# Performance work log

Measured on AMD Instinct MI355X. Metric: run time of the kernel, lower is better.

Reference implementation:

```python
import jax, jax.numpy as jnp
import numpy as np

N_NODES = 100_000
N_EDGES = 3_200_000
N_GRAPHS = 8
HIDDEN = 16
DEPTH = 10
IN_CH = 7  # pos(3)+norm(3)+curve(1); spline=False -> SAGEConv path
EPS = 1e-5
LOC = IN_CH + HIDDEN * DEPTH  # 167
PIN = LOC + 1024              # 1191


def _bn(x, g, b):
    # BatchNorm1d over nodes, training-mode statistics (deterministic)
    m = jnp.mean(x, 0)
    v = jnp.var(x, 0)
    return g * (x - m) * jax.lax.rsqrt(v + EPS) + b


def _sage(x, src, dst, w_nb, b_nb, w_rt):
    # PyG SAGEConv: mean-aggregate neighbor features then linear, plus root linear
    agg = jax.ops.segment_sum(x[src], dst, num_segments=N_NODES)
    cnt = jax.ops.segment_sum(jnp.ones((src.shape[0],), x.dtype), dst, num_segments=N_NODES)
    agg = agg / jnp.maximum(cnt, 1.0)[:, None]
    return agg @ w_nb + b_nb + x @ w_rt


def _mlp_block(x, w, b, g, be):
    # Lin -> ReLU -> BN (dropout is identity in eval mode)
    return _bn(jax.nn.relu(x @ w + b), g, be)


def _forward(pos, norm, curve, edge_index, batch, w_nb0, b_nb0, w_rt0, w_nb, b_nb, w_rt, bn_g, bn_b, g_w1, g_b1, g_g1, g_be1, g_w2, g_b2, g_g2, g_be2, g_w3, g_b3, g_g3, g_be3, p_w1, p_b1, p_g1, p_be1, p_w2, p_b2, p_g2, p_be2, p_w3, p_b3, p_g3, p_be3, out_w, out_b):
    src, dst = edge_index[0], edge_index[1]
    x_sage = jnp.concatenate([pos, norm, curve], axis=1)  # [N, 7]
    x = x_sage
    feats = []
    for i in range(DEPTH):
        if i == 0:
            h = _sage(x, src, dst, w_nb0, b_nb0, w_rt0)
        else:
            h = _sage(x, src, dst, w_nb[i - 1], b_nb[i - 1], w_rt[i - 1])
        x = jax.nn.elu(_bn(h, bn_g[i], bn_b[i]))
        feats.append(x)
    local_features = jnp.concatenate(feats + [x_sage], axis=1)  # [N, 167]
    g = _mlp_block(local_features, g_w1, g_b1, g_g1, g_be1)
    g = _mlp_block(g, g_w2, g_b2, g_g2, g_be2)
    g = _mlp_block(g, g_w3, g_b3, g_g3, g_be3)  # [N, 1024]
    pooled = jax.ops.segment_max(g, batch, num_segments=N_GRAPHS)  # [B, 1024]
    global_features = pooled[batch]  # broadcast back per node (== repeat_interleave)
    p = jnp.concatenate([local_features, global_features], axis=1)  # [N, 1191]
    p = _mlp_block(p, p_w1, p_b1, p_g1, p_be1)
    p = _mlp_block(p, p_w2, p_b2, p_g2, p_be2)
    p = _mlp_block(p, p_w3, p_b3, p_g3, p_be3)
    return p @ out_w + out_b  # [N, 1]


def setup_inputs() -> dict:
    key = jax.random.key(0)
    ks = iter(jax.random.split(key, 64))
    f32 = jnp.float32

    def W(i, o):
        return jax.random.normal(next(ks), (i, o), f32) * (1.0 / np.sqrt(i))

    pos = jax.random.normal(next(ks), (N_NODES, 3), f32)
    norm = jax.random.normal(next(ks), (N_NODES, 3), f32)
    curve = jax.random.normal(next(ks), (N_NODES, 1), f32)
    edge_index = jax.random.randint(next(ks), (2, N_EDGES), 0, N_NODES, dtype=jnp.int32)
    batch = jnp.sort(jax.random.randint(next(ks), (N_NODES,), 0, N_GRAPHS, dtype=jnp.int32))

    w_nb0 = W(IN_CH, HIDDEN); b_nb0 = jnp.zeros((HIDDEN,), f32); w_rt0 = W(IN_CH, HIDDEN)
    w_nb = jax.random.normal(next(ks), (DEPTH - 1, HIDDEN, HIDDEN), f32) * (1.0 / np.sqrt(HIDDEN))
    b_nb = jnp.zeros((DEPTH - 1, HIDDEN), f32)
    w_rt = jax.random.normal(next(ks), (DEPTH - 1, HIDDEN, HIDDEN), f32) * (1.0 / np.sqrt(HIDDEN))
    bn_g = jnp.ones((DEPTH, HIDDEN), f32); bn_b = jnp.zeros((DEPTH, HIDDEN), f32)

    g_w1 = W(LOC, 256); g_b1 = jnp.zeros((256,), f32); g_g1 = jnp.ones((256,), f32); g_be1 = jnp.zeros((256,), f32)
    g_w2 = W(256, 512); g_b2 = jnp.zeros((512,), f32); g_g2 = jnp.ones((512,), f32); g_be2 = jnp.zeros((512,), f32)
    g_w3 = W(512, 1024); g_b3 = jnp.zeros((1024,), f32); g_g3 = jnp.ones((1024,), f32); g_be3 = jnp.zeros((1024,), f32)

    p_w1 = W(PIN, 512); p_b1 = jnp.zeros((512,), f32); p_g1 = jnp.ones((512,), f32); p_be1 = jnp.zeros((512,), f32)
    p_w2 = W(512, 256); p_b2 = jnp.zeros((256,), f32); p_g2 = jnp.ones((256,), f32); p_be2 = jnp.zeros((256,), f32)
    p_w3 = W(256, 128); p_b3 = jnp.zeros((128,), f32); p_g3 = jnp.ones((128,), f32); p_be3 = jnp.zeros((128,), f32)

    out_w = W(128, 1); out_b = jnp.zeros((1,), f32)

    return dict(pos=pos, norm=norm, curve=curve, edge_index=edge_index, batch=batch,
                w_nb0=w_nb0, b_nb0=b_nb0, w_rt0=w_rt0, w_nb=w_nb, b_nb=b_nb, w_rt=w_rt,
                bn_g=bn_g, bn_b=bn_b,
                g_w1=g_w1, g_b1=g_b1, g_g1=g_g1, g_be1=g_be1,
                g_w2=g_w2, g_b2=g_b2, g_g2=g_g2, g_be2=g_be2,
                g_w3=g_w3, g_b3=g_b3, g_g3=g_g3, g_be3=g_be3,
                p_w1=p_w1, p_b1=p_b1, p_g1=p_g1, p_be1=p_be1,
                p_w2=p_w2, p_b2=p_b2, p_g2=p_g2, p_be2=p_be2,
                p_w3=p_w3, p_b3=p_b3, p_g3=p_g3, p_be3=p_be3,
                out_w=out_w, out_b=out_b)


def reference(pos, norm, curve, edge_index, batch, w_nb0, b_nb0, w_rt0, w_nb, b_nb, w_rt, bn_g, bn_b, g_w1, g_b1, g_g1, g_be1, g_w2, g_b2, g_g2, g_be2, g_w3, g_b3, g_g3, g_be3, p_w1, p_b1, p_g1, p_be1, p_w2, p_b2, p_g2, p_be2, p_w3, p_b3, p_g3, p_be3, out_w, out_b):
    return _forward(pos, norm, curve, edge_index, batch, w_nb0, b_nb0, w_rt0, w_nb, b_nb, w_rt, bn_g, bn_b, g_w1, g_b1, g_g1, g_be1, g_w2, g_b2, g_g2, g_be2, g_w3, g_b3, g_g3, g_be3, p_w1, p_b1, p_g1, p_be1, p_w2, p_b2, p_g2, p_be2, p_w3, p_b3, p_g3, p_be3, out_w, out_b)
```

## Files before the change

### kernel.cpp

```cpp
#include <hip/hip_runtime.h>
#include <math.h>

#define NN 100000
#define NE 3200000
#define NGRAPH 8
#define DEPTH 10
#define LOCC 167
#define LOCP 176
#define BNEPS 1e-5f

typedef _Float16 h16;
typedef _Float16 h8 __attribute__((ext_vector_type(8)));
typedef float f4 __attribute__((ext_vector_type(4)));

__device__ __forceinline__ float h2f(h16 v) { return (float)v; }
__device__ __forceinline__ h16 f2h(float v) { return (h16)v; }

__global__ void k_count(const int* __restrict__ dst, int* __restrict__ cnt) {
    int e = blockIdx.x * 256 + threadIdx.x;
    atomicAdd(&cnt[dst[e]], 1);
}

__global__ __launch_bounds__(256) void k_scan1(const int* __restrict__ cnt,
                                               int* __restrict__ row_start,
                                               int* __restrict__ bsum) {
    int i = blockIdx.x * 256 + threadIdx.x;
    int lane = threadIdx.x & 63, wid = threadIdx.x >> 6;
    int v = (i < NN) ? cnt[i] : 0;
    int orig = v;
    #pragma unroll
    for (int off = 1; off < 64; off <<= 1) {
        int u = __shfl_up(v, off, 64);
        if (lane >= off) v += u;
    }
    __shared__ int ws[4];
    if (lane == 63) ws[wid] = v;
    __syncthreads();
    int add = 0;
    for (int w = 0; w < wid; w++) add += ws[w];
    v += add;
    if (i < NN) row_start[i] = v - orig;
    if (threadIdx.x == 255) bsum[blockIdx.x] = v;
}

__global__ __launch_bounds__(512) void k_scan2(int* __restrict__ bsum, int nb) {
    int t = threadIdx.x, lane = t & 63, wid = t >> 6;
    int v = (t < nb) ? bsum[t] : 0;
    int orig = v;
    #pragma unroll
    for (int off = 1; off < 64; off <<= 1) {
        int u = __shfl_up(v, off, 64);
        if (lane >= off) v += u;
    }
    __shared__ int ws[8];
    if (lane == 63) ws[wid] = v;
    __syncthreads();
    int add = 0;
    for (int w = 0; w < wid; w++) add += ws[w];
    v += add;
    if (t < nb) bsum[t] = v - orig;
}

__global__ void k_scan3(const int* __restrict__ cnt, int* __restrict__ row_start,
                        const int* __restrict__ bsum, float* __restrict__ inv_cnt) {
    int i = blockIdx.x * 256 + threadIdx.x;
    if (i < NN) {
        row_start[i] += bsum[blockIdx.x];
        inv_cnt[i] = 1.0f / fmaxf((float)cnt[i], 1.0f);
    }
    if (i == 0) row_start[NN] = NE;
}

__global__ void k_fill(const int* __restrict__ src, const int* __restrict__ dst,
                       const int* __restrict__ row_start, int* __restrict__ cursor,
                       int* __restrict__ csr) {
    int e = blockIdx.x * 256 + threadIdx.x;
    int d = dst[e];
    int o = atomicAdd(&cursor[d], 1);
    csr[row_start[d] + o] = src[e];
}

__global__ void k_build_x0(const float* __restrict__ pos, const float* __restrict__ nrm,
                           const float* __restrict__ cur, float* __restrict__ x,
                           h16* __restrict__ local) {
    int n = blockIdx.x * 256 + threadIdx.x;
    if (n >= NN) return;
    float v[7];
    v[0] = pos[n * 3 + 0]; v[1] = pos[n * 3 + 1]; v[2] = pos[n * 3 + 2];
    v[3] = nrm[n * 3 + 0]; v[4] = nrm[n * 3 + 1]; v[5] = nrm[n * 3 + 2];
    v[6] = cur[n];
    float* xr = x + (size_t)n * 16;
    #pragma unroll
    for (int c = 0; c < 7; c++) xr[c] = v[c];
    #pragma unroll
    for (int c = 7; c < 16; c++) xr[c] = 0.f;
    h16* lr = local + (size_t)n * LOCP;
    #pragma unroll
    for (int c = 0; c < 7; c++) lr[160 + c] = f2h(v[c]);
    #pragma unroll
    for (int c = LOCC; c < LOCP; c++) lr[c] = f2h(0.f);
}

__global__ __launch_bounds__(256) void k_sage(
    const float* __restrict__ x, const int* __restrict__ row_start,
    const int* __restrict__ csr, const float* __restrict__ inv_cnt,
    const float* __restrict__ w_nb, const float* __restrict__ b_nb,
    const float* __restrict__ w_rt, int kin,
    float* __restrict__ h_out, float* __restrict__ ssum, float* __restrict__ ssq) {
    const float4* x4 = (const float4*)x;
    int t = threadIdx.x, lane = t & 63, wid = t >> 6;
    int n = blockIdx.x * 64 + wid * 16 + (lane >> 2);
    int q = lane & 3;
    bool valid = n < NN;
    int s = 0, e = 0;
    if (valid) { s = row_start[n]; e = row_start[n + 1]; }
    float ax = 0.f, ay = 0.f, az = 0.f, aw = 0.f;
    int j = s;
    for (; j + 3 < e; j += 4) {
        int a0 = csr[j], a1 = csr[j + 1], a2 = csr[j + 2], a3 = csr[j + 3];
        float4 v0 = x4[a0 * 4 + q];
        float4 v1 = x4[a1 * 4 + q];
        float4 v2 = x4[a2 * 4 + q];
        float4 v3 = x4[a3 * 4 + q];
        ax += (v0.x + v1.x) + (v2.x + v3.x);
        ay += (v0.y + v1.y) + (v2.y + v3.y);
        az += (v0.z + v1.z) + (v2.z + v3.z);
        aw += (v0.w + v1.w) + (v2.w + v3.w);
    }
    for (; j < e; j++) {
        float4 v = x4[csr[j] * 4 + q];
        ax += v.x; ay += v.y; az += v.z; aw += v.w;
    }
    float ic = valid ? inv_cnt[n] : 0.f;
    float agg[4] = {ax * ic, ay * ic, az * ic, aw * ic};
    float xn[4] = {0.f, 0.f, 0.f, 0.f};
    if (valid) {
        float4 v = x4[n * 4 + q];
        xn[0] = v.x; xn[1] = v.y; xn[2] = v.z; xn[3] = v.w;
    }
    float hc0 = 0.f, hc1 = 0.f, hc2 = 0.f, hc3 = 0.f;
    #pragma unroll
    for (int r = 0; r < 4; r++) {
        int kq = (q + r) & 3;
        int srcl = (lane & 60) | kq;
        float av[4], xv[4];
        #pragma unroll
        for (int c = 0; c < 4; c++) {
            av[c] = __shfl(agg[c], srcl, 64);
            xv[c] = __shfl(xn[c], srcl, 64);
        }
        #pragma unroll
        for (int kk = 0; kk < 4; kk++) {
            int k = kq * 4 + kk;
            if (k < kin) {
                float4 wn4 = *(const float4*)&w_nb[k * 16 + 4 * q];
                float4 wr4 = *(const float4*)&w_rt[k * 16 + 4 * q];
                hc0 = fmaf(av[kk], wn4.x, hc0); hc0 = fmaf(xv[kk], wr4.x, hc0);
                hc1 = fmaf(av[kk], wn4.y, hc1); hc1 = fmaf(xv[kk], wr4.y, hc1);
                hc2 = fmaf(av[kk], wn4.z, hc2); hc2 = fmaf(xv[kk], wr4.z, hc2);
                hc3 = fmaf(av[kk], wn4.w, hc3); hc3 = fmaf(xv[kk], wr4.w, hc3);
            }
        }
    }
    float4 b4 = *(const float4*)&b_nb[4 * q];
    hc0 += b4.x; hc1 += b4.y; hc2 += b4.z; hc3 += b4.w;
    if (!valid) { hc0 = 0.f; hc1 = 0.f; hc2 = 0.f; hc3 = 0.f; }
    else {
        *(float4*)&h_out[(size_t)n * 16 + 4 * q] = make_float4(hc0, hc1, hc2, hc3);
    }
    float s0 = hc0, s1 = hc1, s2 = hc2, s3 = hc3;
    float q0 = hc0 * hc0, q1 = hc1 * hc1, q2 = hc2 * hc2, q3 = hc3 * hc3;
    #pragma unroll
    for (int off = 4; off < 64; off <<= 1) {
        s0 += __shfl_xor(s0, off, 64); s1 += __shfl_xor(s1, off, 64);
        s2 += __shfl_xor(s2, off, 64); s3 += __shfl_xor(s3, off, 64);
        q0 += __shfl_xor(q0, off, 64); q1 += __shfl_xor(q1, off, 64);
        q2 += __shfl_xor(q2, off, 64); q3 += __shfl_xor(q3, off, 64);
    }
    if (lane < 4) {
        int slot = blockIdx.x & 63;
        float* ps = &ssum[slot * 16 + 4 * lane];
        float* pq = &ssq[slot * 16 + 4 * lane];
        atomicAdd(ps + 0, s0); atomicAdd(ps + 1, s1);
        atomicAdd(ps + 2, s2); atomicAdd(ps + 3, s3);
        atomicAdd(pq + 0, q0); atomicAdd(pq + 1, q1);
        atomicAdd(pq + 2, q2); atomicAdd(pq + 3, q3);
    }
}

__global__ void k_bn_fin(float* __restrict__ ssum, float* __restrict__ ssq,
                         const float* __restrict__ g, const float* __restrict__ b,
                         float M, int C, float* __restrict__ scale, float* __restrict__ shift) {
    int c = blockIdx.x * blockDim.x + threadIdx.x;
    if (c >= C) return;
    float s = 0.f, q = 0.f;
    for (int sl = 0; sl < 64; sl++) {
        s += ssum[sl * C + c]; ssum[sl * C + c] = 0.f;
        q += ssq[sl * C + c];  ssq[sl * C + c] = 0.f;
    }
    float mean = s / M;
    float var = q / M - mean * mean;
    var = var > 0.f ? var : 0.f;
    float sc = g[c] / sqrtf(var + BNEPS);
    scale[c] = sc;
    shift[c] = b[c] - mean * sc;
}

__global__ void k_apply(const float* __restrict__ h, const float* __restrict__ scale,
                        const float* __restrict__ shift, float* __restrict__ x,
                        h16* __restrict__ local, int colbase) {
    int t = blockIdx.x * 256 + threadIdx.x;
    int n = t >> 4, c = t & 15;
    float v = fmaf(h[t], scale[c], shift[c]);
    float e = v > 0.f ? v : expm1f(v);
    x[t] = e;
    local[(size_t)n * LOCP + colbase + c] = f2h(e);
}

__global__ void k_wt(const float* __restrict__ W, const float* __restrict__ scale,
                     h16* __restrict__ WtH, h16* __restrict__ WtL,
                     int N, int Kin, int Kpad, int split, int gap) {
    int u = blockIdx.x * 256 + threadIdx.x;
    int nkc = Kpad >> 5;
    int total = (N >> 4) * nkc * 64;
    if (u >= total) return;
    int lane = u & 63;
    int fc = u >> 6;
    int kc = fc % nkc;
    int cs = fc / nkc;
    int col = cs * 16 + (lane & 15);
    int kbase = kc * 32 + ((lane >> 4) << 3);
    h8 hh, ll;
    #pragma unroll
    for (int j = 0; j < 8; j++) {
        int k = kbase + j;
        float v = 0.f;
        int kr = (k < split) ? k : (k - gap);
        bool valid = (k < split) ? (k < Kin) : (k >= split + gap && kr < Kin);
        if (valid) {
            v = W[(size_t)kr * N + col];
            if (scale) v *= scale[kr];
        }
        h16 hi = f2h(v);
        hh[j] = hi;
        ll[j] = f2h(v - h2f(hi));
    }
    *(h8*)(WtH + (size_t)u * 8) = hh;
    *(h8*)(WtL + (size_t)u * 8) = ll;
}

__global__ void k_bias2(const float* __restrict__ W, const float* __restrict__ bias,
                        const float* __restrict__ shift, float* __restrict__ bias2,
                        int N, int Kin) {
    int n = blockIdx.x;
    int lane = threadIdx.x;
    float acc = 0.f;
    if (shift) {
        for (int k = lane; k < Kin; k += 64)
            acc = fmaf(shift[k], W[(size_t)k * N + n], acc);
    }
    for (int off = 32; off; off >>= 1) acc += __shfl_down(acc, off, 64);
    if (lane == 0) bias2[n] = bias[n] + acc;
}

template <bool CONCAT, bool POOL>
__global__ __launch_bounds__(256) void k_gemm(
    const h16* __restrict__ A, int lda, int KA,
    const h16* __restrict__ WtH, const h16* __restrict__ WtL, int Kpad,
    const float* __restrict__ bias2, int Nc,
    const h16* __restrict__ Gp, const int* __restrict__ batch,
    int M,
    h16* __restrict__ C,
    float* __restrict__ ssum, float* __restrict__ ssq,
    unsigned* __restrict__ mx, unsigned* __restrict__ mn) {
    __shared__ h16 As[2][2048];

    const int t = threadIdx.x;
    const int row0 = blockIdx.y * 64;
    const int col0 = blockIdx.x * 128;
    const int w = t >> 6, lane = t & 63, quad = lane >> 4, m = lane & 15;
    const int nkc = Kpad >> 5;

    f4 acc[2][4];
    #pragma unroll
    for (int sp = 0; sp < 2; sp++)
        #pragma unroll
        for (int i = 0; i < 4; i++)
            #pragma unroll
            for (int j = 0; j < 4; j++) acc[sp][i][j] = 0.f;

    const int rl = ((t >> 6) << 4) | (t & 15);
    const int ch = (t >> 4) & 3;
    const int r = row0 + rl;
    int bg = 0;
    if (CONCAT) bg = (r < M) ? batch[r] : 0;
    const h16* Arow = A + (size_t)r * lda;
    const int st = t * 8;
    const int fidx = quad * 128 + m * 8;
    size_t bo0 = ((size_t)((col0 >> 4) + w) * nkc * 64 + lane) * 8;
    size_t bo1 = ((size_t)((col0 >> 4) + w + 4) * nkc * 64 + lane) * 8;

    auto LOADA = [&](int k0, h8& av) {
        int k = k0 + ch * 8;
        #pragma unroll
        for (int j = 0; j < 8; j++) av[j] = (h16)0.f;
        if (r < M) {
            if (!CONCAT) {
                if (k < KA) av = *(const h8*)(Arow + k);
            } else {
                if (k < LOCP) av = *(const h8*)(Arow + k);
                else if (k < KA) av = *(const h8*)(Gp + (size_t)bg * 1024 + (k - LOCP));
            }
        }
    };

    h8 a0, a1;
    h8 cbh0, cbl0, cbh1, cbl1, nbh0, nbl0, nbh1, nbl1;
    LOADA(0, a0);
    cbh0 = *(const h8*)(WtH + bo0); cbl0 = *(const h8*)(WtL + bo0);
    cbh1 = *(const h8*)(WtH + bo1); cbl1 = *(const h8*)(WtL + bo1);

    for (int kt = 0; kt < nkc; kt++) {
        h16* buf = (h16*)As[kt & 1];
        *(h8*)(buf + st) = a0;
        if (kt + 1 < nkc) {
            LOADA((kt + 1) * 32, a1);
            size_t o0 = bo0 + (size_t)(kt + 1) * 512;
            size_t o1 = bo1 + (size_t)(kt + 1) * 512;
            nbh0 = *(const h8*)(WtH + o0); nbl0 = *(const h8*)(WtL + o0);
            nbh1 = *(const h8*)(WtH + o1); nbl1 = *(const h8*)(WtL + o1);
        }
        __syncthreads();
        #pragma unroll
        for (int rt = 0; rt < 4; rt++) {
            h8 af = *(const h8*)(buf + rt * 512 + fidx);
            acc[0][rt] = __builtin_amdgcn_mfma_f32_16x16x32_f16(af, cbh0, acc[0][rt], 0, 0, 0);
            acc[0][rt] = __builtin_amdgcn_mfma_f32_16x16x32_f16(af, cbl0, acc[0][rt], 0, 0, 0);
            acc[1][rt] = __builtin_amdgcn_mfma_f32_16x16x32_f16(af, cbh1, acc[1][rt], 0, 0, 0);
            acc[1][rt] = __builtin_amdgcn_mfma_f32_16x16x32_f16(af, cbl1, acc[1][rt], 0, 0, 0);
        }
        a0 = a1;
        cbh0 = nbh0; cbl0 = nbl0; cbh1 = nbh1; cbl1 = nbl1;
    }

    bool unig = true; int gblk = 0;
    if (POOL) {
        gblk = batch[min(row0, M - 1)];
        unig = (batch[min(row0 + 63, M - 1)] == gblk);
    }

    #pragma unroll
    for (int sp = 0; sp < 2; sp++) {
        const int col = col0 + (w + 4 * sp) * 16 + m;
        const float bi = bias2[col];
        float sv = 0.f, qv = 0.f;
        unsigned um = 0u, un = 0x7f800000u;
        #pragma unroll
        for (int rt = 0; rt < 4; rt++) {
            #pragma unroll
            for (int rg = 0; rg < 4; rg++) {
                int rr = row0 + rt * 16 + quad * 4 + rg;
                if (rr < M) {
                    float y = acc[sp][rt][rg] + bi;
                    y = y > 0.f ? y : 0.f;
                    if (!POOL) C[(size_t)rr * Nc + col] = f2h(y);
                    sv += y; qv += y * y;
                    if (POOL) {
                        unsigned ub = __float_as_uint(y);
                        if (unig) { um = max(um, ub); un = min(un, ub); }
                        else {
                            int gg = batch[rr];
                            atomicMax(&mx[gg * 1024 + col], ub);
                            atomicMin(&mn[gg * 1024 + col], ub);
                        }
                    }
                }
            }
        }
        sv += __shfl_xor(sv, 16, 64); sv += __shfl_xor(sv, 32, 64);
        qv += __shfl_xor(qv, 16, 64); qv += __shfl_xor(qv, 32, 64);
        if (POOL && unig) {
            um = max(um, (unsigned)__shfl_xor((int)um, 16, 64));
            um = max(um, (unsigned)__shfl_xor((int)um, 32, 64));
            un = min(un, (unsigned)__shfl_xor((int)un, 16, 64));
            un = min(un, (unsigned)__shfl_xor((int)un, 32, 64));
        }
        if (quad == 0) {
            int slot = blockIdx.y & 63;
            atomicAdd(&ssum[slot * Nc + col], sv);
            atomicAdd(&ssq[slot * Nc + col], qv);
            if (POOL && unig) {
                atomicMax(&mx[gblk * 1024 + col], um);
                atomicMin(&mn[gblk * 1024 + col], un);
            }
        }
    }
}

__global__ void k_init_minmax(unsigned* __restrict__ mx, unsigned* __restrict__ mn) {
    int i = blockIdx.x * 256 + threadIdx.x;
    if (i < NGRAPH * 1024) { mx[i] = 0u; mn[i] = 0x7f800000u; }
}

__global__ void k_pool_fin(const unsigned* __restrict__ mx, const unsigned* __restrict__ mn,
                           const float* __restrict__ scale, const float* __restrict__ shift,
                           h16* __restrict__ pooled_h) {
    int i = blockIdx.x * 256 + threadIdx.x;
    if (i >= NGRAPH * 1024) return;
    int c = i & 1023;
    float sc = scale[c], sh = shift[c];
    float vmax = __uint_as_float(mx[i]);
    float vmin = __uint_as_float(mn[i]);
    float v = sc > 0.f ? fmaf(sc, vmax, sh) : fmaf(sc, vmin, sh);
    pooled_h[i] = f2h(v);
}

__global__ void k_fold(const float* __restrict__ scale, const float* __restrict__ shift,
                       const float* __restrict__ ow, const float* __restrict__ ob,
                       float* __restrict__ wprime, float* __restrict__ bprime) {
    int c = threadIdx.x;
    float w = ow[c];
    wprime[c] = scale[c] * w;
    float v = shift[c] * w;
    for (int off = 32; off; off >>= 1) v += __shfl_down(v, off, 64);
    __shared__ float l[2];
    if ((c & 63) == 0) l[c >> 6] = v;
    __syncthreads();
    if (c == 0) bprime[0] = l[0] + l[1] + ob[0];
}

__global__ void k_out(const h16* __restrict__ p3, const float* __restrict__ wprime,
                      const float* __restrict__ bprime, float* __restrict__ out) {
    int n = blockIdx.x * 256 + threadIdx.x;
    if (n >= NN) return;
    const h16* r = p3 + (size_t)n * 128;
    float acc = bprime[0];
    #pragma unroll
    for (int q = 0; q < 128; q++) acc = fmaf(h2f(r[q]), wprime[q], acc);
    out[n] = acc;
}

extern "C" void kernel_launch(void* const* d_in, const int* in_sizes, int n_in,
                              void* d_out, int out_size, void* d_ws, size_t ws_size,
                              hipStream_t stream) {
    const float* pos = (const float*)d_in[0];
    const float* nrm = (const float*)d_in[1];
    const float* cur = (const float*)d_in[2];
    const int* ei = (const int*)d_in[3];
    const int* src = ei;
    const int* dst = ei + NE;
    const int* batch = (const int*)d_in[4];
    const float* w_nb0 = (const float*)d_in[5];
    const float* b_nb0 = (const float*)d_in[6];
    const float* w_rt0 = (const float*)d_in[7];
    const float* w_nb = (const float*)d_in[8];
    const float* b_nb = (const float*)d_in[9];
    const float* w_rt = (const float*)d_in[10];
    const float* bn_g = (const float*)d_in[11];
    const float* bn_b = (const float*)d_in[12];
    const float* g_w1 = (const float*)d_in[13];
    const float* g_b1 = (const float*)d_in[14];
    const float* g_g1 = (const float*)d_in[15];
    const float* g_be1 = (const float*)d_in[16];
    const float* g_w2 = (const float*)d_in[17];
    const float* g_b2 = (const float*)d_in[18];
    const float* g_g2 = (const float*)d_in[19];
    const float* g_be2 = (const float*)d_in[20];
    const float* g_w3 = (const float*)d_in[21];
    const float* g_b3 = (const float*)d_in[22];
    const float* g_g3 = (const float*)d_in[23];
    const float* g_be3 = (const float*)d_in[24];
    const float* p_w1 = (const float*)d_in[25];
    const float* p_b1 = (const float*)d_in[26];
    const float* p_g1 = (const float*)d_in[27];
    const float* p_be1 = (const float*)d_in[28];
    const float* p_w2 = (const float*)d_in[29];
    const float* p_b2 = (const float*)d_in[30];
    const float* p_g2 = (const float*)d_in[31];
    const float* p_be2 = (const float*)d_in[32];
    const float* p_w3 = (const float*)d_in[33];
    const float* p_b3 = (const float*)d_in[34];
    const float* p_g3 = (const float*)d_in[35];
    const float* p_be3 = (const float*)d_in[36];
    const float* out_w = (const float*)d_in[37];
    const float* out_b = (const float*)d_in[38];
    float* out = (float*)d_out;

    char* base = (char*)d_ws;
    size_t off = 0;
    auto alloc = [&](size_t bytes) -> void* {
        void* p = base + off;
        off = (off + bytes + 255) & ~(size_t)255;
        return p;
    };

    int* cnt = (int*)alloc((size_t)NN * 4);
    int* cursor = (int*)alloc((size_t)NN * 4);
    float* sg_sum = (float*)alloc(64 * 16 * 4);
    float* sg_sq = (float*)alloc(64 * 16 * 4);
    int* row_start = (int*)alloc((size_t)(NN + 1) * 4);
    float* inv_cnt = (float*)alloc((size_t)NN * 4);
    int* bsum = (int*)alloc(512 * 4);
    h16* wt_arena = (h16*)base;
    h16* WtH_g1 = wt_arena + 0;
    h16* WtH_g2 = wt_arena + 49152;
    h16* WtH_g3 = wt_arena + 180224;
    h16* WtH_p1 = wt_arena + 0;
    h16* WtH_p2 = wt_arena + 622592;
    h16* WtH_p3 = wt_arena + 753664;

    float* gs_sum = (float*)alloc(64 * 1024 * 4);
    float* gs_sq = (float*)alloc(64 * 1024 * 4);
    size_t zend = off;

    h16* wtlo_arena = (h16*)alloc((size_t)786432 * 2);
    h16* WtL_g1 = wtlo_arena + 0;
    h16* WtL_g2 = wtlo_arena + 49152;
    h16* WtL_g3 = wtlo_arena + 180224;
    h16* WtL_p1 = wtlo_arena + 0;
    h16* WtL_p2 = wtlo_arena + 622592;
    h16* WtL_p3 = wtlo_arena + 753664;

    float* sage_scale = (float*)alloc(DEPTH * 16 * 4);
    float* sage_shift = (float*)alloc(DEPTH * 16 * 4);
    const int CS[6] = {256, 512, 1024, 512, 256, 128};
    float* sc_arr[6];
    float* sh_arr[6];
    for (int i = 0; i < 6; i++) {
        sc_arr[i] = (float*)alloc(CS[i] * 4);
        sh_arr[i] = (float*)alloc(CS[i] * 4);
    }
    unsigned* mx = (unsigned*)alloc(NGRAPH * 1024 * 4);
    unsigned* mn = (unsigned*)alloc(NGRAPH * 1024 * 4);
    h16* pooled_h = (h16*)alloc(NGRAPH * 1024 * 2);
    float* wprime = (float*)alloc(128 * 4);
    float* bprime = (float*)alloc(256);
    float* bias2 = (float*)alloc(2688 * 4);
    float* b2_g1 = bias2 + 0;
    float* b2_g2 = bias2 + 256;
    float* b2_g3 = bias2 + 768;
    float* b2_p1 = bias2 + 1792;
    float* b2_p2 = bias2 + 2304;
    float* b2_p3 = bias2 + 2560;

    h16* local = (h16*)alloc((size_t)NN * LOCP * 2);

    size_t O = off;
    float* x_cur = (float*)(base + O);
    float* h_buf = (float*)(base + O + (size_t)NN * 64);
    int* csr = (int*)(base + O + (size_t)NN * 128);
    h16* g1b = (h16*)(base + O);
    h16* g2b = (h16*)(base + O + (size_t)NN * 512);
    h16* p1b = g2b;
    h16* p2b = g1b;
    h16* p3b = local;
    size_t need = O + (size_t)NN * 512 + (size_t)NN * 1024;

    if (need > ws_size) return;

    const int NB = (NN + 255) / 256;
    hipMemsetAsync(base, 0, zend, stream);
    k_init_minmax<<<32, 256, 0, stream>>>(mx, mn);
    k_count<<<NE / 256, 256, 0, stream>>>(dst, cnt);
    k_scan1<<<NB, 256, 0, stream>>>(cnt, row_start, bsum);
    k_scan2<<<1, 512, 0, stream>>>(bsum, NB);
    k_scan3<<<NB, 256, 0, stream>>>(cnt, row_start, bsum, inv_cnt);
    k_fill<<<NE / 256, 256, 0, stream>>>(src, dst, row_start, cursor, csr);
    k_build_x0<<<(NN + 255) / 256, 256, 0, stream>>>(pos, nrm, cur, x_cur, local);

    for (int i = 0; i < DEPTH; i++) {
        const float* wn = (i == 0) ? w_nb0 : (w_nb + (size_t)(i - 1) * 256);
        const float* bnb = (i == 0) ? b_nb0 : (b_nb + (size_t)(i - 1) * 16);
        const float* wr = (i == 0) ? w_rt0 : (w_rt + (size_t)(i - 1) * 256);
        int kin = (i == 0) ? 7 : 16;
        k_sage<<<(NN + 63) / 64, 256, 0, stream>>>(x_cur, row_start, csr, inv_cnt,
                                                   wn, bnb, wr, kin, h_buf, sg_sum, sg_sq);
        k_bn_fin<<<1, 64, 0, stream>>>(sg_sum, sg_sq, bn_g + i * 16, bn_b + i * 16,
                                       (float)NN, 16, sage_scale + i * 16, sage_shift + i * 16);
        k_apply<<<NN * 16 / 256, 256, 0, stream>>>(h_buf, sage_scale + i * 16,
                                                   sage_shift + i * 16, x_cur, local, i * 16);
    }

    const int GRY = (NN + 63) / 64;

    k_wt<<<(256 * 192 / 8 + 255) / 256, 256, 0, stream>>>(g_w1, nullptr, WtH_g1, WtL_g1, 256, 167, 192, 167, 0);
    k_bias2<<<256, 64, 0, stream>>>(g_w1, g_b1, nullptr, b2_g1, 256, 167);
    k_gemm<false, false><<<dim3(2, GRY), 256, 0, stream>>>(
        local, LOCP, LOCP, WtH_g1, WtL_g1, 192, b2_g1, 256, nullptr, batch, NN,
        g1b, gs_sum, gs_sq, nullptr, nullptr);
    k_bn_fin<<<1, 256, 0, stream>>>(gs_sum, gs_sq, g_g1, g_be1, (float)NN, 256, sc_arr[0], sh_arr[0]);

    k_wt<<<(512 * 256 / 8 + 255) / 256, 256, 0, stream>>>(g_w2, sc_arr[0], WtH_g2, WtL_g2, 512, 256, 256, 256, 0);
    k_bias2<<<512, 64, 0, stream>>>(g_w2, g_b2, sh_arr[0], b2_g2, 512, 256);
    k_gemm<false, false><<<dim3(4, GRY), 256, 0, stream>>>(
        g1b, 256, 256, WtH_g2, WtL_g2, 256, b2_g2, 512, nullptr, batch, NN,
        g2b, gs_sum, gs_sq, nullptr, nullptr);
    k_bn_fin<<<2, 256, 0, stream>>>(gs_sum, gs_sq, g_g2, g_be2, (float)NN, 512, sc_arr[1], sh_arr[1]);

    k_wt<<<(1024 * 512 / 8 + 255) / 256, 256, 0, stream>>>(g_w3, sc_arr[1], WtH_g3, WtL_g3, 1024, 512, 512, 512, 0);
    k_bias2<<<1024, 64, 0, stream>>>(g_w3, g_b3, sh_arr[1], b2_g3, 1024, 512);
    k_gemm<false, true><<<dim3(8, GRY), 256, 0, stream>>>(
        g2b, 512, 512, WtH_g3, WtL_g3, 512, b2_g3, 1024, nullptr, batch, NN,
        nullptr, gs_sum, gs_sq, mx, mn);
    k_bn_fin<<<4, 256, 0, stream>>>(gs_sum, gs_sq, g_g3, g_be3, (float)NN, 1024, sc_arr[2], sh_arr[2]);
    k_pool_fin<<<32, 256, 0, stream>>>(mx, mn, sc_arr[2], sh_arr[2], pooled_h);

    k_wt<<<(512 * 1216 / 8 + 255) / 256, 256, 0, stream>>>(p_w1, nullptr, WtH_p1, WtL_p1, 512, 1191, 1216, 167, 9);
    k_bias2<<<512, 64, 0, stream>>>(p_w1, p_b1, nullptr, b2_p1, 512, 1191);
    k_gemm<true, false><<<dim3(4, GRY), 256, 0, stream>>>(
        local, LOCP, 1200, WtH_p1, WtL_p1, 1216, b2_p1, 512, pooled_h, batch, NN,
        p1b, gs_sum, gs_sq, nullptr, nullptr);
    k_bn_fin<<<2, 256, 0, stream>>>(gs_sum, gs_sq, p_g1, p_be1, (float)NN, 512, sc_arr[3], sh_arr[3]);

    k_wt<<<(256 * 512 / 8 + 255) / 256, 256, 0, stream>>>(p_w2, sc_arr[3], WtH_p2, WtL_p2, 256, 512, 512, 512, 0);
    k_bias2<<<256, 64, 0, stream>>>(p_w2, p_b2, sh_arr[3], b2_p2, 256, 512);
    k_gemm<false, false><<<dim3(2, GRY), 256, 0, stream>>>(
        p1b, 512, 512, WtH_p2, WtL_p2, 512, b2_p2, 256, nullptr, batch, NN,
        p2b, gs_sum, gs_sq, nullptr, nullptr);
    k_bn_fin<<<1, 256, 0, stream>>>(gs_sum, gs_sq, p_g2, p_be2, (float)NN, 256, sc_arr[4], sh_arr[4]);

    k_wt<<<(128 * 256 / 8 + 255) / 256, 256, 0, stream>>>(p_w3, sc_arr[4], WtH_p3, WtL_p3, 128, 256, 256, 256, 0);
    k_bias2<<<128, 64, 0, stream>>>(p_w3, p_b3, sh_arr[4], b2_p3, 128, 256);
    k_gemm<false, false><<<dim3(1, GRY), 256, 0, stream>>>(
        p2b, 256, 256, WtH_p3, WtL_p3, 256, b2_p3, 128, nullptr, batch, NN,
        p3b, gs_sum, gs_sq, nullptr, nullptr);
    k_bn_fin<<<1, 128, 0, stream>>>(gs_sum, gs_sq, p_g3, p_be3, (float)NN, 128, sc_arr[5], sh_arr[5]);

    k_fold<<<1, 128, 0, stream>>>(sc_arr[5], sh_arr[5], out_w, out_b, wprime, bprime);
    k_out<<<(NN + 255) / 256, 256, 0, stream>>>(p3b, wprime, bprime, out);
}
```

Baseline: 1.995 ms.

## Widen GEMM column tiles, fuse BN finalize into apply, unroll SAGE gather

The GEMM kernel is templated on the number of 64-column subtiles per block, and most layers now use 256 columns per block, so each A tile staged in LDS is reused across more output columns. BN finalize for the SAGE layers is folded into k_apply, which recomputes scale and shift per block from per-layer partial sums. Those partial-sum buffers are sized per layer so no zeroing pass is needed. The neighbour gather loop is unrolled by 8 with two accumulator sets to keep more loads in flight. The wider tiles raise register pressure and halve the block count, which can hurt occupancy.

```diff
diff --git a/kernel.cpp b/kernel.cpp
--- a/kernel.cpp
+++ b/kernel.cpp
@@ -115,22 +115,33 @@
     int s = 0, e = 0;
     if (valid) { s = row_start[n]; e = row_start[n + 1]; }
     float ax = 0.f, ay = 0.f, az = 0.f, aw = 0.f;
+    float bx = 0.f, by = 0.f, bz = 0.f, bw = 0.f;
     int j = s;
-    for (; j + 3 < e; j += 4) {
+    for (; j + 7 < e; j += 8) {
         int a0 = csr[j], a1 = csr[j + 1], a2 = csr[j + 2], a3 = csr[j + 3];
+        int a4 = csr[j + 4], a5 = csr[j + 5], a6 = csr[j + 6], a7 = csr[j + 7];
         float4 v0 = x4[a0 * 4 + q];
         float4 v1 = x4[a1 * 4 + q];
         float4 v2 = x4[a2 * 4 + q];
         float4 v3 = x4[a3 * 4 + q];
+        float4 v4 = x4[a4 * 4 + q];
+        float4 v5 = x4[a5 * 4 + q];
+        float4 v6 = x4[a6 * 4 + q];
+        float4 v7 = x4[a7 * 4 + q];
         ax += (v0.x + v1.x) + (v2.x + v3.x);
         ay += (v0.y + v1.y) + (v2.y + v3.y);
         az += (v0.z + v1.z) + (v2.z + v3.z);
         aw += (v0.w + v1.w) + (v2.w + v3.w);
+        bx += (v4.x + v5.x) + (v6.x + v7.x);
+        by += (v4.y + v5.y) + (v6.y + v7.y);
+        bz += (v4.z + v5.z) + (v6.z + v7.z);
+        bw += (v4.w + v5.w) + (v6.w + v7.w);
     }
     for (; j < e; j++) {
         float4 v = x4[csr[j] * 4 + q];
         ax += v.x; ay += v.y; az += v.z; aw += v.w;
     }
+    ax += bx; ay += by; az += bz; aw += bw;
     float ic = valid ? inv_cnt[n] : 0.f;
     float agg[4] = {ax * ic, ay * ic, az * ic, aw * ic};
     float xn[4] = {0.f, 0.f, 0.f, 0.f};
@@ -188,6 +199,34 @@
     }
 }
 
+__global__ void k_apply(const float* __restrict__ h,
+                        const float* __restrict__ ssum, const float* __restrict__ ssq,
+                        const float* __restrict__ g, const float* __restrict__ b,
+                        float* __restrict__ x, h16* __restrict__ local, int colbase) {
+    __shared__ float sscale[16], sshift[16];
+    int t = threadIdx.x;
+    if (t < 16) {
+        float s = 0.f, q = 0.f;
+        for (int sl = 0; sl < 64; sl++) {
+            s += ssum[sl * 16 + t];
+            q += ssq[sl * 16 + t];
+        }
+        float mean = s / (float)NN;
+        float var = q / (float)NN - mean * mean;
+        var = var > 0.f ? var : 0.f;
+        float sc = g[t] / sqrtf(var + BNEPS);
+        sscale[t] = sc;
+        sshift[t] = b[t] - mean * sc;
+    }
+    __syncthreads();
+    int i = blockIdx.x * 256 + t;
+    int n = i >> 4, c = i & 15;
+    float v = fmaf(h[i], sscale[c], sshift[c]);
+    float e = v > 0.f ? v : expm1f(v);
+    x[i] = e;
+    local[(size_t)n * LOCP + colbase + c] = f2h(e);
+}
+
 __global__ void k_bn_fin(float* __restrict__ ssum, float* __restrict__ ssq,
                          const float* __restrict__ g, const float* __restrict__ b,
                          float M, int C, float* __restrict__ scale, float* __restrict__ shift) {
@@ -204,17 +243,6 @@
     float sc = g[c] / sqrtf(var + BNEPS);
     scale[c] = sc;
     shift[c] = b[c] - mean * sc;
-}
-
-__global__ void k_apply(const float* __restrict__ h, const float* __restrict__ scale,
-                        const float* __restrict__ shift, float* __restrict__ x,
-                        h16* __restrict__ local, int colbase) {
-    int t = blockIdx.x * 256 + threadIdx.x;
-    int n = t >> 4, c = t & 15;
-    float v = fmaf(h[t], scale[c], shift[c]);
-    float e = v > 0.f ? v : expm1f(v);
-    x[t] = e;
-    local[(size_t)n * LOCP + colbase + c] = f2h(e);
 }
 
 __global__ void k_wt(const float* __restrict__ W, const float* __restrict__ scale,
@@ -263,7 +291,7 @@
     if (lane == 0) bias2[n] = bias[n] + acc;
 }
 
-template <bool CONCAT, bool POOL>
+template <int NS, bool CONCAT, bool POOL>
 __global__ __launch_bounds__(256) void k_gemm(
     const h16* __restrict__ A, int lda, int KA,
     const h16* __restrict__ WtH, const h16* __restrict__ WtL, int Kpad,
@@ -277,13 +305,13 @@
 
     const int t = threadIdx.x;
     const int row0 = blockIdx.y * 64;
-    const int col0 = blockIdx.x * 128;
+    const int col0 = blockIdx.x * (NS * 64);
     const int w = t >> 6, lane = t & 63, quad = lane >> 4, m = lane & 15;
     const int nkc = Kpad >> 5;
 
-    f4 acc[2][4];
-    #pragma unroll
-    for (int sp = 0; sp < 2; sp++)
+    f4 acc[NS][4];
+    #pragma unroll
+    for (int sp = 0; sp < NS; sp++)
         #pragma unroll
         for (int i = 0; i < 4; i++)
             #pragma unroll
@@ -297,8 +325,10 @@
     const h16* Arow = A + (size_t)r * lda;
     const int st = t * 8;
     const int fidx = quad * 128 + m * 8;
-    size_t bo0 = ((size_t)((col0 >> 4) + w) * nkc * 64 + lane) * 8;
-    size_t bo1 = ((size_t)((col0 >> 4) + w + 4) * nkc * 64 + lane) * 8;
+    size_t bo[NS];
+    #pragma unroll
+    for (int sp = 0; sp < NS; sp++)
+        bo[sp] = ((size_t)((col0 >> 4) + w + 4 * sp) * nkc * 64 + lane) * 8;
 
     auto LOADA = [&](int k0, h8& av) {
         int k = k0 + ch * 8;
@@ -315,32 +345,39 @@
     };
 
     h8 a0, a1;
-    h8 cbh0, cbl0, cbh1, cbl1, nbh0, nbl0, nbh1, nbl1;
+    h8 cbh[NS], cbl[NS], nbh[NS], nbl[NS];
     LOADA(0, a0);
-    cbh0 = *(const h8*)(WtH + bo0); cbl0 = *(const h8*)(WtL + bo0);
-    cbh1 = *(const h8*)(WtH + bo1); cbl1 = *(const h8*)(WtL + bo1);
+    #pragma unroll
+    for (int sp = 0; sp < NS; sp++) {
+        cbh[sp] = *(const h8*)(WtH + bo[sp]);
+        cbl[sp] = *(const h8*)(WtL + bo[sp]);
+    }
 
     for (int kt = 0; kt < nkc; kt++) {
         h16* buf = (h16*)As[kt & 1];
         *(h8*)(buf + st) = a0;
         if (kt + 1 < nkc) {
             LOADA((kt + 1) * 32, a1);
-            size_t o0 = bo0 + (size_t)(kt + 1) * 512;
-            size_t o1 = bo1 + (size_t)(kt + 1) * 512;
-            nbh0 = *(const h8*)(WtH + o0); nbl0 = *(const h8*)(WtL + o0);
-            nbh1 = *(const h8*)(WtH + o1); nbl1 = *(const h8*)(WtL + o1);
+            #pragma unroll
+            for (int sp = 0; sp < NS; sp++) {
+                size_t o = bo[sp] + (size_t)(kt + 1) * 512;
+                nbh[sp] = *(const h8*)(WtH + o);
+                nbl[sp] = *(const h8*)(WtL + o);
+            }
         }
         __syncthreads();
         #pragma unroll
         for (int rt = 0; rt < 4; rt++) {
             h8 af = *(const h8*)(buf + rt * 512 + fidx);
-            acc[0][rt] = __builtin_amdgcn_mfma_f32_16x16x32_f16(af, cbh0, acc[0][rt], 0, 0, 0);
-            acc[0][rt] = __builtin_amdgcn_mfma_f32_16x16x32_f16(af, cbl0, acc[0][rt], 0, 0, 0);
-            acc[1][rt] = __builtin_amdgcn_mfma_f32_16x16x32_f16(af, cbh1, acc[1][rt], 0, 0, 0);
-            acc[1][rt] = __builtin_amdgcn_mfma_f32_16x16x32_f16(af, cbl1, acc[1][rt], 0, 0, 0);
+            #pragma unroll
+            for (int sp = 0; sp < NS; sp++) {
+                acc[sp][rt] = __builtin_amdgcn_mfma_f32_16x16x32_f16(af, cbh[sp], acc[sp][rt], 0, 0, 0);
+                acc[sp][rt] = __builtin_amdgcn_mfma_f32_16x16x32_f16(af, cbl[sp], acc[sp][rt], 0, 0, 0);
+            }
         }
         a0 = a1;
-        cbh0 = nbh0; cbl0 = nbl0; cbh1 = nbh1; cbl1 = nbl1;
+        #pragma unroll
+        for (int sp = 0; sp < NS; sp++) { cbh[sp] = nbh[sp]; cbl[sp] = nbl[sp]; }
     }
 
     bool unig = true; int gblk = 0;
@@ -350,7 +387,7 @@
     }
 
     #pragma unroll
-    for (int sp = 0; sp < 2; sp++) {
+    for (int sp = 0; sp < NS; sp++) {
         const int col = col0 + (w + 4 * sp) * 16 + m;
         const float bi = bias2[col];
         float sv = 0.f, qv = 0.f;
@@ -496,8 +533,8 @@
 
     int* cnt = (int*)alloc((size_t)NN * 4);
     int* cursor = (int*)alloc((size_t)NN * 4);
-    float* sg_sum = (float*)alloc(64 * 16 * 4);
-    float* sg_sq = (float*)alloc(64 * 16 * 4);
+    float* sg_sum = (float*)alloc(DEPTH * 64 * 16 * 4);
+    float* sg_sq = (float*)alloc(DEPTH * 64 * 16 * 4);
     int* row_start = (int*)alloc((size_t)(NN + 1) * 4);
     float* inv_cnt = (float*)alloc((size_t)NN * 4);
     int* bsum = (int*)alloc(512 * 4);
@@ -521,8 +558,6 @@
     h16* WtL_p2 = wtlo_arena + 622592;
     h16* WtL_p3 = wtlo_arena + 753664;
 
-    float* sage_scale = (float*)alloc(DEPTH * 16 * 4);
-    float* sage_shift = (float*)alloc(DEPTH * 16 * 4);
     const int CS[6] = {256, 512, 1024, 512, 256, 128};
     float* sc_arr[6];
     float* sh_arr[6];
@@ -573,33 +608,33 @@
         const float* bnb = (i == 0) ? b_nb0 : (b_nb + (size_t)(i - 1) * 16);
         const float* wr = (i == 0) ? w_rt0 : (w_rt + (size_t)(i - 1) * 256);
         int kin = (i == 0) ? 7 : 16;
+        float* ls = sg_sum + i * 1024;
+        float* lq = sg_sq + i * 1024;
         k_sage<<<(NN + 63) / 64, 256, 0, stream>>>(x_cur, row_start, csr, inv_cnt,
-                                                   wn, bnb, wr, kin, h_buf, sg_sum, sg_sq);
-        k_bn_fin<<<1, 64, 0, stream>>>(sg_sum, sg_sq, bn_g + i * 16, bn_b + i * 16,
-                                       (float)NN, 16, sage_scale + i * 16, sage_shift + i * 16);
-        k_apply<<<NN * 16 / 256, 256, 0, stream>>>(h_buf, sage_scale + i * 16,
-                                                   sage_shift + i * 16, x_cur, local, i * 16);
+                                                   wn, bnb, wr, kin, h_buf, ls, lq);
+        k_apply<<<NN * 16 / 256, 256, 0, stream>>>(h_buf, ls, lq, bn_g + i * 16, bn_b + i * 16,
+                                                   x_cur, local, i * 16);
     }
 
     const int GRY = (NN + 63) / 64;
 
     k_wt<<<(256 * 192 / 8 + 255) / 256, 256, 0, stream>>>(g_w1, nullptr, WtH_g1, WtL_g1, 256, 167, 192, 167, 0);
     k_bias2<<<256, 64, 0, stream>>>(g_w1, g_b1, nullptr, b2_g1, 256, 167);
-    k_gemm<false, false><<<dim3(2, GRY), 256, 0, stream>>>(
+    k_gemm<4, false, false><<<dim3(1, GRY), 256, 0, stream>>>(
         local, LOCP, LOCP, WtH_g1, WtL_g1, 192, b2_g1, 256, nullptr, batch, NN,
         g1b, gs_sum, gs_sq, nullptr, nullptr);
     k_bn_fin<<<1, 256, 0, stream>>>(gs_sum, gs_sq, g_g1, g_be1, (float)NN, 256, sc_arr[0], sh_arr[0]);
 
     k_wt<<<(512 * 256 / 8 + 255) / 256, 256, 0, stream>>>(g_w2, sc_arr[0], WtH_g2, WtL_g2, 512, 256, 256, 256, 0);
     k_bias2<<<512, 64, 0, stream>>>(g_w2, g_b2, sh_arr[0], b2_g2, 512, 256);
-    k_gemm<false, false><<<dim3(4, GRY), 256, 0, stream>>>(
+    k_gemm<4, false, false><<<dim3(2, GRY), 256, 0, stream>>>(
         g1b, 256, 256, WtH_g2, WtL_g2, 256, b2_g2, 512, nullptr, batch, NN,
         g2b, gs_sum, gs_sq, nullptr, nullptr);
     k_bn_fin<<<2, 256, 0, stream>>>(gs_sum, gs_sq, g_g2, g_be2, (float)NN, 512, sc_arr[1], sh_arr[1]);
 
     k_wt<<<(1024 * 512 / 8 + 255) / 256, 256, 0, stream>>>(g_w3, sc_arr[1], WtH_g3, WtL_g3, 1024, 512, 512, 512, 0);
     k_bias2<<<1024, 64, 0, stream>>>(g_w3, g_b3, sh_arr[1], b2_g3, 1024, 512);
-    k_gemm<false, true><<<dim3(8, GRY), 256, 0, stream>>>(
+    k_gemm<4, false, true><<<dim3(4, GRY), 256, 0, stream>>>(
         g2b, 512, 512, WtH_g3, WtL_g3, 512, b2_g3, 1024, nullptr, batch, NN,
         nullptr, gs_sum, gs_sq, mx, mn);
     k_bn_fin<<<4, 256, 0, stream>>>(gs_sum, gs_sq, g_g3, g_be3, (float)NN, 1024, sc_arr[2], sh_arr[2]);
@@ -607,21 +642,21 @@
 
     k_wt<<<(512 * 1216 / 8 + 255) / 256, 256, 0, stream>>>(p_w1, nullptr, WtH_p1, WtL_p1, 512, 1191, 1216, 167, 9);
     k_bias2<<<512, 64, 0, stream>>>(p_w1, p_b1, nullptr, b2_p1, 512, 1191);
-    k_gemm<true, false><<<dim3(4, GRY), 256, 0, stream>>>(
+    k_gemm<4, true, false><<<dim3(2, GRY), 256, 0, stream>>>(
         local, LOCP, 1200, WtH_p1, WtL_p1, 1216, b2_p1, 512, pooled_h, batch, NN,
         p1b, gs_sum, gs_sq, nullptr, nullptr);
     k_bn_fin<<<2, 256, 0, stream>>>(gs_sum, gs_sq, p_g1, p_be1, (float)NN, 512, sc_arr[3], sh_arr[3]);
 
     k_wt<<<(256 * 512 / 8 + 255) / 256, 256, 0, stream>>>(p_w2, sc_arr[3], WtH_p2, WtL_p2, 256, 512, 512, 512, 0);
     k_bias2<<<256, 64, 0, stream>>>(p_w2, p_b2, sh_arr[3], b2_p2, 256, 512);
-    k_gemm<false, false><<<dim3(2, GRY), 256, 0, stream>>>(
+    k_gemm<4, false, false><<<dim3(1, GRY), 256, 0, stream>>>(
         p1b, 512, 512, WtH_p2, WtL_p2, 512, b2_p2, 256, nullptr, batch, NN,
         p2b, gs_sum, gs_sq, nullptr, nullptr);
     k_bn_fin<<<1, 256, 0, stream>>>(gs_sum, gs_sq, p_g2, p_be2, (float)NN, 256, sc_arr[4], sh_arr[4]);
 
     k_wt<<<(128 * 256 / 8 + 255) / 256, 256, 0, stream>>>(p_w3, sc_arr[4], WtH_p3, WtL_p3, 128, 256, 256, 256, 0);
     k_bias2<<<128, 64, 0, stream>>>(p_w3, p_b3, sh_arr[4], b2_p3, 128, 256);
-    k_gemm<false, false><<<dim3(1, GRY), 256, 0, stream>>>(
+    k_gemm<2, false, false><<<dim3(1, GRY), 256, 0, stream>>>(
         p2b, 256, 256, WtH_p3, WtL_p3, 256, b2_p3, 128, nullptr, batch, NN,
         p3b, gs_sum, gs_sq, nullptr, nullptr);
     k_bn_fin<<<1, 128, 0, stream>>>(gs_sum, gs_sq, p_g3, p_be3, (float)NN, 128, sc_arr[5], sh_arr[5]);
```

Result: slower. 2.141 ms (+7.4%).
